# Kernel optimization log

Hardware: AMD Instinct MI355X
Metric: run time of the kernel (lower is better)

The kernel has to match this reference:

```python
import jax, jax.numpy as jnp
import numpy as np

N = 50000   # nodes
E = 600000  # edges (time_feat is per-edge: same mask indexes k and src_idx)
D = 128     # adapter_dim
C = 8       # num_clusters
SCALE = D ** -0.5


def setup_inputs() -> dict:
    key = jax.random.key(0)
    ks = jax.random.split(key, 12)
    s = 1.0 / np.sqrt(D)
    return {
        "node_feat": jax.random.normal(ks[0], (N, D), jnp.float32),
        "time_feat": jax.random.normal(ks[1], (E, D), jnp.float32),
        "context_feat": jax.random.normal(ks[2], (N, D), jnp.float32),
        "edge_index": jax.random.randint(ks[3], (2, E), 0, N),
        "Wq": jax.random.uniform(ks[4], (D, D), jnp.float32, -s, s),
        "bq": jnp.zeros((D,), jnp.float32),
        "Wk": jax.random.uniform(ks[5], (D, D), jnp.float32, -s, s),
        "bk": jnp.zeros((D,), jnp.float32),
        "Wv": jax.random.uniform(ks[6], (D, D), jnp.float32, -s, s),
        "bv": jnp.zeros((D,), jnp.float32),
        "cluster_emb": jax.random.normal(ks[7], (C, D), jnp.float32),
        "Wo": jax.random.uniform(ks[8], (D, D), jnp.float32, -s, s),
        "bo": jnp.zeros((D,), jnp.float32),
    }


def reference(node_feat, time_feat, context_feat, edge_index,
              Wq, bq, Wk, bk, Wv, bv, cluster_emb, Wo, bo):
    q = node_feat @ Wq + bq            # [N, D]
    k = time_feat @ Wk + bk            # [E, D]
    v = time_feat @ Wv + bv            # [E, D]

    # cluster routing: argmax(softmax(sim)) == argmax(sim)
    sim = (time_feat @ cluster_emb.T) * SCALE   # [E, C]
    assign = jnp.argmax(sim, axis=-1)           # [E] int

    src = edge_index[0]                          # [E]
    seg = assign * N + src                       # combined (cluster, dst-of-scatter) segment id
    nseg = C * N

    attn = jnp.sum(q[src] * k, axis=-1) * SCALE  # [E]

    # scatter_softmax per (cluster, src node)
    seg_max = jax.ops.segment_max(attn, seg, num_segments=nseg)
    ex = jnp.exp(attn - seg_max[seg])
    denom = jax.ops.segment_sum(ex, seg, num_segments=nseg)
    w = ex / denom[seg]                          # [E]

    # scatter_mean per (cluster, src node) -> [C, N, D]
    wv = v * w[:, None]
    sums = jax.ops.segment_sum(wv, seg, num_segments=nseg)                 # [C*N, D]
    counts = jax.ops.segment_sum(jnp.ones((E,), v.dtype), seg, num_segments=nseg)
    means = sums / jnp.maximum(counts, 1.0)[:, None]                       # empty -> 0
    per_cluster = means.reshape(C, N, D)

    # sum(outputs) / len(outputs): only non-empty clusters contribute an entry
    edges_per_cluster = jax.ops.segment_sum(jnp.ones((E,), jnp.float32), assign, num_segments=C)
    num_nonempty = jnp.sum((edges_per_cluster > 0).astype(jnp.float32))
    combined = per_cluster.sum(axis=0) / num_nonempty                      # [N, D]

    return jax.nn.relu(combined @ Wo + bo)
```

## Files before the change

### kernel.cpp

```cpp
#include <hip/hip_runtime.h>
#include <math.h>


#define NN 50000
#define NE 600000
#define DD 128
#define NC 8
#define WIN 64
#define NWIN 9376
#define NBF  9377
#define EC 70
#define NLOC 32
#define SCALEF 0.08838834764831845f

#define OFF_NODECNT  0
#define OFF_FILL     50000
#define OFF_MASK     100000
#define ZERO_ELEMS   100256
#define OFF_NODEOFF  100352
#define OFF_PARTIAL  150352
#define OFF_BF       150608
#define OFF_BQK      160000
#define OFF_BVO      160128
#define OFF_WQBK     160256
#define OFF_C0       160384
#define OFF_WQK      160400
#define OFF_WVO      176784
#define OFF_QB       193168
#define OFF_SORTED   243168
#define OFF_SRCS     843168
#define OFF_SW       1443168
#define OFF_P        1493168

__device__ __forceinline__ float dot4(float4 a, float4 b) {
  return a.x * b.x + a.y * b.y + a.z * b.z + a.w * b.w;
}

__global__ __launch_bounds__(256) void k_pre_count(
    const float* __restrict__ Wq, const float* __restrict__ bq,
    const float* __restrict__ Wk, const float* __restrict__ bk,
    const float* __restrict__ Wv, const float* __restrict__ bv,
    const float* __restrict__ Wo, const int* __restrict__ ei,
    int* __restrict__ node_cnt,
    float* __restrict__ Wqk, float* __restrict__ bqk,
    float* __restrict__ Wvo, float* __restrict__ bvo,
    float* __restrict__ wqbk, float* __restrict__ c0) {
  int bid = blockIdx.x, t = threadIdx.x;
  if (bid >= 129) {
    long e = (long)(bid - 129) * 256 + t;
    if (e < NE) atomicAdd(&node_cnt[ei[e]], 1);
    return;
  }
  __shared__ float rq[DD], rv[DD];
  int b = bid;
  if (b < DD) {
    if (t < DD) { rq[t] = Wq[b * DD + t]; rv[t] = Wv[b * DD + t]; }
    __syncthreads();
    if (t < DD) {
      float aq = 0.f, av = 0.f;
      for (int j = 0; j < DD; j++) {
        aq += rq[j] * Wk[t * DD + j];
        av += rv[j] * Wo[j * DD + t];
      }
      Wqk[b * DD + t] = aq;
      Wvo[b * DD + t] = av;
    }
  } else {
    if (t < DD) {
      float a1 = 0.f, a2 = 0.f, a3 = 0.f;
      for (int j = 0; j < DD; j++) {
        a1 += bq[j] * Wk[t * DD + j];
        a2 += bv[j] * Wo[j * DD + t];
        a3 += Wq[t * DD + j] * bk[j];
      }
      bqk[t] = a1; bvo[t] = a2; wqbk[t] = a3;
      if (t == 0) {
        float s = 0.f;
        for (int j = 0; j < DD; j++) s += bq[j] * bk[j];
        *c0 = s;
      }
    }
  }
}

__global__ __launch_bounds__(256) void k_p(
    const float* __restrict__ nf, const float* __restrict__ Wqk,
    const float* __restrict__ bqk, const float* __restrict__ wqbk,
    const float* __restrict__ c0p,
    float* __restrict__ p, float* __restrict__ qb) {
  __shared__ float a_lds[64 * DD];
  __shared__ float wb_lds[DD];
  int t = threadIdx.x;
  long row0 = (long)blockIdx.x * 64;
  for (int it = 0; it < 8; it++) {
    int idx = (it * 256 + t) * 4;
    long r = row0 + idx / DD;
    float4 v = {0.f, 0.f, 0.f, 0.f};
    if (r < NN) v = *(const float4*)(nf + r * DD + (idx % DD));
    *(float4*)(a_lds + idx) = v;
  }
  if (t < DD) wb_lds[t] = wqbk[t];
  __syncthreads();
  int cg = t % 32, rg = t / 32;
  int col0 = cg * 4, r0 = rg * 8;
  float acc[8][4]; float qacc[8];
  for (int r = 0; r < 8; r++) { qacc[r] = 0.f; for (int c = 0; c < 4; c++) acc[r][c] = 0.f; }
  for (int k = 0; k < DD; k++) {
    float4 b4 = *(const float4*)(Wqk + k * DD + col0);
    float wbk = wb_lds[k];
    for (int r = 0; r < 8; r++) {
      float a = a_lds[(r0 + r) * DD + k];
      acc[r][0] += a * b4.x; acc[r][1] += a * b4.y;
      acc[r][2] += a * b4.z; acc[r][3] += a * b4.w;
      qacc[r] += a * wbk;
    }
  }
  float4 bq4 = *(const float4*)(bqk + col0);
  float c0v = *c0p;
  for (int r = 0; r < 8; r++) {
    long row = row0 + r0 + r;
    if (row < NN) {
      float4 o;
      o.x = acc[r][0] + bq4.x; o.y = acc[r][1] + bq4.y;
      o.z = acc[r][2] + bq4.z; o.w = acc[r][3] + bq4.w;
      *(float4*)(p + row * DD + col0) = o;
      if (cg == 0) qb[row] = qacc[r] + c0v;
    }
  }
}

__global__ __launch_bounds__(256) void k_scan1(const int* __restrict__ node_cnt,
                                               int* __restrict__ partial) {
  int i = blockIdx.x * 256 + threadIdx.x;
  int v = (i < NN) ? node_cnt[i] : 0;
  for (int o = 1; o < 64; o <<= 1) v += __shfl_xor(v, o);
  __shared__ int wsum[4];
  if ((threadIdx.x & 63) == 0) wsum[threadIdx.x >> 6] = v;
  __syncthreads();
  if (threadIdx.x == 0) partial[blockIdx.x] = wsum[0] + wsum[1] + wsum[2] + wsum[3];
}

__global__ __launch_bounds__(256) void k_scan2(int* __restrict__ partial) {
  __shared__ int s[256];
  int t = threadIdx.x;
  int v = (t < 196) ? partial[t] : 0;
  s[t] = v;
  __syncthreads();
  for (int o = 1; o < 256; o <<= 1) {
    int add = (t >= o) ? s[t - o] : 0;
    __syncthreads();
    s[t] += add;
    __syncthreads();
  }
  if (t < 196) partial[t] = s[t] - v;
}

__global__ __launch_bounds__(256) void k_scan3(const int* __restrict__ node_cnt,
                                               const int* __restrict__ partial,
                                               int* __restrict__ node_off) {
  __shared__ int s[256];
  int t = threadIdx.x;
  int i = blockIdx.x * 256 + t;
  int v = (i < NN) ? node_cnt[i] : 0;
  s[t] = v;
  __syncthreads();
  for (int o = 1; o < 256; o <<= 1) {
    int add = (t >= o) ? s[t - o] : 0;
    __syncthreads();
    s[t] += add;
    __syncthreads();
  }
  if (i < NN) node_off[i] = partial[blockIdx.x] + s[t] - v;
}

#define EDGE_BLKS 2344
#define BS_BLKS   37
__global__ __launch_bounds__(256) void k_scatter(const int* __restrict__ ei,
                                                 const int* __restrict__ node_off,
                                                 int* __restrict__ fill,
                                                 int* __restrict__ sorted,
                                                 int* __restrict__ srcs,
                                                 int* __restrict__ blockFirst) {
  int bid = blockIdx.x, t = threadIdx.x;
  if (bid >= EDGE_BLKS) {
    int w = (bid - EDGE_BLKS) * 256 + t;
    if (w < NBF) {
      int v = w * WIN, lo = 0, hi = NN;
      while (lo < hi) { int mid = (lo + hi) >> 1; if (node_off[mid] < v) lo = mid + 1; else hi = mid; }
      blockFirst[w] = lo;
    }
    return;
  }
  long e = (long)bid * 256 + t;
  if (e < NE) {
    int s = ei[e];
    int pos = node_off[s] + atomicAdd(&fill[s], 1);
    sorted[pos] = (int)e;
    srcs[pos] = s;
  }
}

__device__ __forceinline__ void phase_a16(
    const float* __restrict__ tf, const float* __restrict__ p,
    const float4 (&ceg)[NC][2], float* t_lds, float* exf_sh, int* cli_sh,
    float* D_sh, int* C_sh,
    int slot, int jA, int eid, int src, int lnode, float qbv,
    bool doStage, bool doDC) {
  const float* trow = tf + (long)eid * DD;
  float4 t0 = *(const float4*)(trow + jA * 4);
  float4 t1 = *(const float4*)(trow + (16 + jA) * 4);
  if (doStage) {
    int e7 = slot & 7;
    *(float4*)(t_lds + slot * DD + ((jA ^ e7) << 2)) = t0;
    *(float4*)(t_lds + slot * DD + ((16 + (jA ^ e7)) << 2)) = t1;
  }
  const float* prow = p + (long)src * DD;
  float4 p0 = *(const float4*)(prow + jA * 4);
  float4 p1 = *(const float4*)(prow + (16 + jA) * 4);
  float a = dot4(t0, p0) + dot4(t1, p1);
  float sims[NC];
  #pragma unroll
  for (int c = 0; c < NC; c++)
    sims[c] = dot4(t0, ceg[c][0]) + dot4(t1, ceg[c][1]);
  #pragma unroll
  for (int c = 0; c < NC; c++) {
    sims[c] += __shfl_xor(sims[c], 1);
    sims[c] += __shfl_xor(sims[c], 2);
    sims[c] += __shfl_xor(sims[c], 4);
    sims[c] += __shfl_xor(sims[c], 8);
  }
  a += __shfl_xor(a, 1);
  a += __shfl_xor(a, 2);
  a += __shfl_xor(a, 4);
  a += __shfl_xor(a, 8);
  if (jA == 0) {
    float best = sims[0]; int bc = 0;
    #pragma unroll
    for (int c = 1; c < NC; c++) if (sims[c] > best) { best = sims[c]; bc = c; }
    float ex = expf((a + qbv) * SCALEF);
    exf_sh[slot] = ex; cli_sh[slot] = bc;
    if (doDC) {
      atomicAdd(&D_sh[lnode * NC + bc], ex);
      atomicAdd(&C_sh[lnode * NC + bc], 1);
    }
  }
}

__global__ __launch_bounds__(256, 4) void k_fused5(
    const float* __restrict__ tf, const int* __restrict__ sorted,
    const int* __restrict__ srcs, const int* __restrict__ node_off,
    const int* __restrict__ node_cnt, const int* __restrict__ blockFirst,
    const float* __restrict__ ce, const float* __restrict__ p,
    const float* __restrict__ qb, int* __restrict__ maskArr,
    float* __restrict__ agg, float* __restrict__ sw) {
  __shared__ float t_lds[EC * DD];
  __shared__ float exf_sh[EC];
  __shared__ float scl_sh[EC];
  __shared__ int   cli_sh[EC];
  __shared__ int   eidx_sh[EC];
  __shared__ int   srcs_sh[EC];
  __shared__ int   offL_sh[NLOC];
  __shared__ int   cntL_sh[NLOC];
  __shared__ float qb_sh[NLOC];
  __shared__ float D_sh[NLOC * NC];
  __shared__ int   C_sh[NLOC * NC];
  __shared__ int   ctrl[4];

  int t = threadIdx.x, b = blockIdx.x;
  int fn = blockFirst[b], ln = blockFirst[b + 1] - 1;
  if (fn >= NN || ln < fn) return;

  int elA = t >> 4, jA = t & 15;
  int team = t >> 5, c4 = t & 31;
  int msk = 0;

  float4 ceg[NC][2];
  #pragma unroll
  for (int c = 0; c < NC; c++) {
    ceg[c][0] = *(const float4*)(ce + c * DD + jA * 4);
    ceg[c][1] = *(const float4*)(ce + c * DD + (16 + jA) * 4);
  }

  int s0 = fn;
  while (s0 <= ln) {
    if (t < 64) {
      int offv = 0, cntv = 0; bool fit = false;
      bool valid = (t < NLOC && s0 + t <= ln);
      if (valid) { offv = node_off[s0 + t]; cntv = node_cnt[s0 + t]; }
      int off0 = __shfl(offv, 0);
      if (valid) {
        fit = (offv - off0 + cntv) <= EC;
        offL_sh[t] = offv - off0; cntL_sh[t] = cntv; qb_sh[t] = qb[s0 + t];
      }
      unsigned long long bm = __ballot(fit);
      int pref = (int)__popcll(bm);
      if (t == 0) { ctrl[0] = pref; ctrl[2] = off0; }
      if (pref > 0 && t == pref - 1) ctrl[1] = offv - off0 + cntv;
    }
    for (int i = t; i < NLOC * NC; i += 256) { D_sh[i] = 0.f; C_sh[i] = 0; }
    __syncthreads();
    int nN = ctrl[0], eb = ctrl[2];

    if (nN == 0) {
      int cnt = cntL_sh[0];
      float qbv0 = qb_sh[0];
      for (int c0 = 0; c0 < cnt; c0 += 16) {
        int el = c0 + elA;
        if (el < cnt)
          phase_a16(tf, p, ceg, t_lds, exf_sh, cli_sh, D_sh, C_sh,
                    elA, jA, sorted[eb + el], s0, 0, qbv0, false, true);
      }
      __syncthreads();
      float4 r = {0.f, 0.f, 0.f, 0.f};
      for (int c0 = 0; c0 < cnt; c0 += EC) {
        int m = cnt - c0; if (m > EC) m = EC;
        for (int r0 = 0; r0 < m; r0 += 16) {
          int sl = r0 + elA;
          if (sl < m)
            phase_a16(tf, p, ceg, t_lds, exf_sh, cli_sh, D_sh, C_sh,
                      sl, jA, sorted[eb + c0 + sl], s0, 0, qbv0, true, false);
        }
        __syncthreads();
        if (t < m) {
          int c = cli_sh[t];
          scl_sh[t] = exf_sh[t] * __builtin_amdgcn_rcpf(D_sh[c] * (float)C_sh[c]);
        }
        __syncthreads();
        for (int e = team; e < m; e += 8) {
          float s = scl_sh[e];
          const float4 tv = *(const float4*)(t_lds + e * DD + ((c4 ^ (e & 7)) << 2));
          r.x += s * tv.x; r.y += s * tv.y; r.z += s * tv.z; r.w += s * tv.w;
        }
        __syncthreads();
      }
      *(float4*)(t_lds + team * DD + c4 * 4) = r;
      __syncthreads();
      if (t < DD) {
        float acc = 0.f;
        #pragma unroll
        for (int tm = 0; tm < 8; tm++) acc += t_lds[tm * DD + t];
        agg[(long)s0 * DD + t] = acc;
      }
      if (t == 0) {
        float ssw = 0.f; int mk = 0;
        #pragma unroll
        for (int c = 0; c < NC; c++) {
          int cc = C_sh[c];
          if (cc > 0) { mk |= 1 << c; ssw += __builtin_amdgcn_rcpf((float)cc); }
        }
        sw[s0] = ssw; msk |= mk;
      }
      __syncthreads();
      s0 += 1;
      continue;
    }

    int span = ctrl[1];

    if (t < span) { eidx_sh[t] = sorted[eb + t]; srcs_sh[t] = srcs[eb + t]; }
    __syncthreads();

    float4 tc0 = {0.f,0.f,0.f,0.f}, tc1 = {0.f,0.f,0.f,0.f};
    if (elA < span) {
      const float* tr = tf + (long)eidx_sh[elA] * DD;
      tc0 = *(const float4*)(tr + jA * 4);
      tc1 = *(const float4*)(tr + (16 + jA) * 4);
    }
    for (int r0 = 0; r0 < span; r0 += 16) {
      int el = r0 + elA;
      int eln = el + 16;
      float4 tn0 = {0.f,0.f,0.f,0.f}, tn1 = {0.f,0.f,0.f,0.f};
      if (eln < span) {
        const float* tr = tf + (long)eidx_sh[eln] * DD;
        tn0 = *(const float4*)(tr + jA * 4);
        tn1 = *(const float4*)(tr + (16 + jA) * 4);
      }
      if (el < span) {
        int src = srcs_sh[el];
        int e7 = el & 7;
        *(float4*)(t_lds + el * DD + ((jA ^ e7) << 2)) = tc0;
        *(float4*)(t_lds + el * DD + ((16 + (jA ^ e7)) << 2)) = tc1;
        const float* prow = p + (long)src * DD;
        float4 p0 = *(const float4*)(prow + jA * 4);
        float4 p1 = *(const float4*)(prow + (16 + jA) * 4);
        float a = dot4(tc0, p0) + dot4(tc1, p1);
        float sims[NC];
        #pragma unroll
        for (int c = 0; c < NC; c++)
          sims[c] = dot4(tc0, ceg[c][0]) + dot4(tc1, ceg[c][1]);
        #pragma unroll
        for (int c = 0; c < NC; c++) {
          sims[c] += __shfl_xor(sims[c], 1);
          sims[c] += __shfl_xor(sims[c], 2);
          sims[c] += __shfl_xor(sims[c], 4);
          sims[c] += __shfl_xor(sims[c], 8);
        }
        a += __shfl_xor(a, 1);
        a += __shfl_xor(a, 2);
        a += __shfl_xor(a, 4);
        a += __shfl_xor(a, 8);
        if (jA == 0) {
          float best = sims[0]; int bc = 0;
          #pragma unroll
          for (int c = 1; c < NC; c++) if (sims[c] > best) { best = sims[c]; bc = c; }
          float ex = expf((a + qb_sh[src - s0]) * SCALEF);
          exf_sh[el] = ex; cli_sh[el] = bc;
          atomicAdd(&D_sh[(src - s0) * NC + bc], ex);
          atomicAdd(&C_sh[(src - s0) * NC + bc], 1);
        }
      }
      tc0 = tn0; tc1 = tn1;
    }
    __syncthreads();

    if (t < span) {
      int l = (srcs_sh[t] - s0) * NC + cli_sh[t];
      scl_sh[t] = exf_sh[t] * __builtin_amdgcn_rcpf(D_sh[l] * (float)C_sh[l]);
    }
    __syncthreads();

    for (int k = team; k < nN; k += 8) {
      float4 r = {0.f, 0.f, 0.f, 0.f};
      int e1 = offL_sh[k] + cntL_sh[k];
      for (int e = offL_sh[k]; e < e1; e++) {
        float s = scl_sh[e];
        const float4 tv = *(const float4*)(t_lds + e * DD + ((c4 ^ (e & 7)) << 2));
        r.x += s * tv.x; r.y += s * tv.y; r.z += s * tv.z; r.w += s * tv.w;
      }
      long n = s0 + k;
      *(float4*)(agg + n * DD + c4 * 4) = r;
      if (c4 == 0) {
        float ssw = 0.f; int mk = 0;
        #pragma unroll
        for (int c = 0; c < NC; c++) {
          int cc = C_sh[k * NC + c];
          if (cc > 0) { mk |= 1 << c; ssw += __builtin_amdgcn_rcpf((float)cc); }
        }
        sw[n] = ssw; msk |= mk;
      }
    }
    __syncthreads();
    s0 += nN;
  }
  if ((t & 31) == 0 && msk) atomicOr(&maskArr[b & 255], msk);
}

__global__ __launch_bounds__(256) void k_out(
    const float* __restrict__ agg, const float* __restrict__ Wvo,
    const float* __restrict__ bvo, const float* __restrict__ sw,
    const float* __restrict__ bo, const int* __restrict__ maskArr,
    float* __restrict__ out) {
  __shared__ float a_lds[64 * DD];
  __shared__ float sw_lds[64];
  __shared__ int morw[4];
  int t = threadIdx.x;
  int mv = maskArr[t];
  for (int o = 1; o < 64; o <<= 1) mv |= __shfl_xor(mv, o);
  if ((t & 63) == 0) morw[t >> 6] = mv;
  long row0 = (long)blockIdx.x * 64;
  for (int it = 0; it < 8; it++) {
    int idx = (it * 256 + t) * 4;
    long r = row0 + idx / DD;
    float4 v = {0.f, 0.f, 0.f, 0.f};
    if (r < NN) v = *(const float4*)(agg + r * DD + (idx % DD));
    *(float4*)(a_lds + idx) = v;
  }
  if (t < 64) {
    long r = row0 + t;
    sw_lds[t] = (r < NN) ? sw[r] : 0.f;
  }
  __syncthreads();
  int full = morw[0] | morw[1] | morw[2] | morw[3];
  int nne = __popc(full); if (nne == 0) nne = 1;
  float inv = 1.0f / (float)nne;
  int cg = t % 32, rg = t / 32;
  int col0 = cg * 4, r0 = rg * 8;
  float acc[8][4];
  for (int r = 0; r < 8; r++) for (int c = 0; c < 4; c++) acc[r][c] = 0.f;
  for (int k = 0; k < DD; k++) {
    float4 b4 = *(const float4*)(Wvo + k * DD + col0);
    for (int r = 0; r < 8; r++) {
      float a = a_lds[(r0 + r) * DD + k];
      acc[r][0] += a * b4.x; acc[r][1] += a * b4.y;
      acc[r][2] += a * b4.z; acc[r][3] += a * b4.w;
    }
  }
  float4 bv4 = *(const float4*)(bvo + col0);
  float4 bo4 = *(const float4*)(bo + col0);
  for (int r = 0; r < 8; r++) {
    long row = row0 + r0 + r;
    if (row < NN) {
      float s = sw_lds[r0 + r];
      float4 o;
      o.x = fmaxf((acc[r][0] + s * bv4.x) * inv + bo4.x, 0.f);
      o.y = fmaxf((acc[r][1] + s * bv4.y) * inv + bo4.y, 0.f);
      o.z = fmaxf((acc[r][2] + s * bv4.z) * inv + bo4.z, 0.f);
      o.w = fmaxf((acc[r][3] + s * bv4.w) * inv + bo4.w, 0.f);
      *(float4*)(out + row * DD + col0) = o;
    }
  }
}

extern "C" void kernel_launch(void* const* d_in, const int* in_sizes, int n_in,
                              void* d_out, int out_size, void* d_ws, size_t ws_size,
                              hipStream_t stream) {
  const float* nf = (const float*)d_in[0];
  const float* tf = (const float*)d_in[1];
  const int*   ei = (const int*)d_in[3];
  const float* Wq = (const float*)d_in[4];
  const float* bq = (const float*)d_in[5];
  const float* Wk = (const float*)d_in[6];
  const float* bk = (const float*)d_in[7];
  const float* Wv = (const float*)d_in[8];
  const float* bv = (const float*)d_in[9];
  const float* ce = (const float*)d_in[10];
  const float* Wo = (const float*)d_in[11];
  const float* bo = (const float*)d_in[12];
  float* out = (float*)d_out;

  float* ws  = (float*)d_ws;
  int*   node_cnt = (int*)(ws + OFF_NODECNT);
  int*   fill     = (int*)(ws + OFF_FILL);
  int*   maskArr  = (int*)(ws + OFF_MASK);
  int*   node_off = (int*)(ws + OFF_NODEOFF);
  int*   partial  = (int*)(ws + OFF_PARTIAL);
  int*   blockFirst = (int*)(ws + OFF_BF);
  float* bqk      = ws + OFF_BQK;
  float* bvo      = ws + OFF_BVO;
  float* wqbk     = ws + OFF_WQBK;
  float* c0       = ws + OFF_C0;
  float* Wqk      = ws + OFF_WQK;
  float* Wvo      = ws + OFF_WVO;
  float* qb       = ws + OFF_QB;
  int*   sorted   = (int*)(ws + OFF_SORTED);
  int*   srcs     = (int*)(ws + OFF_SRCS);
  float* sw       = ws + OFF_SW;
  float* p        = ws + OFF_P;
  float* agg      = ws + OFF_P;

  hipMemsetAsync(d_ws, 0, (size_t)ZERO_ELEMS * 4, stream);

  k_pre_count<<<129 + EDGE_BLKS, 256, 0, stream>>>(
      Wq, bq, Wk, bk, Wv, bv, Wo, ei, node_cnt, Wqk, bqk, Wvo, bvo, wqbk, c0);
  k_p<<<(NN + 63) / 64, 256, 0, stream>>>(nf, Wqk, bqk, wqbk, c0, p, qb);
  k_scan1<<<196, 256, 0, stream>>>(node_cnt, partial);
  k_scan2<<<1, 256, 0, stream>>>(partial);
  k_scan3<<<196, 256, 0, stream>>>(node_cnt, partial, node_off);
  k_scatter<<<EDGE_BLKS + BS_BLKS, 256, 0, stream>>>(ei, node_off, fill, sorted,
                                                     srcs, blockFirst);
  k_fused5<<<NWIN, 256, 0, stream>>>(tf, sorted, srcs, node_off, node_cnt,
                                     blockFirst, ce, p, qb, maskArr, agg, sw);
  k_out<<<(NN + 63) / 64, 256, 0, stream>>>(agg, Wvo, bvo, sw, bo, maskArr, out);
}
```

Before: 666.0 us.

## Stage all edge time-feature rows into LDS upfront and shrink edge windows

```diff
diff --git a/kernel.cpp b/kernel.cpp
--- a/kernel.cpp
+++ b/kernel.cpp
@@ -6,11 +6,11 @@
 #define NE 600000
 #define DD 128
 #define NC 8
-#define WIN 64
-#define NWIN 9376
-#define NBF  9377
+#define WIN 56
+#define NWIN 10715
+#define NBF  10716
 #define EC 70
-#define NLOC 32
+#define NLOC 24
 #define SCALEF 0.08838834764831845f
 
 #define OFF_NODECNT  0
@@ -20,17 +20,17 @@
 #define OFF_NODEOFF  100352
 #define OFF_PARTIAL  150352
 #define OFF_BF       150608
-#define OFF_BQK      160000
-#define OFF_BVO      160128
-#define OFF_WQBK     160256
-#define OFF_C0       160384
-#define OFF_WQK      160400
-#define OFF_WVO      176784
-#define OFF_QB       193168
-#define OFF_SORTED   243168
-#define OFF_SRCS     843168
-#define OFF_SW       1443168
-#define OFF_P        1493168
+#define OFF_BQK      161328
+#define OFF_BVO      161456
+#define OFF_WQBK     161584
+#define OFF_C0       161712
+#define OFF_WQK      161728
+#define OFF_WVO      178112
+#define OFF_QB       194496
+#define OFF_SORTED   244496
+#define OFF_SRCS     844496
+#define OFF_SW       1444496
+#define OFF_P        1494496
 
 __device__ __forceinline__ float dot4(float4 a, float4 b) {
   return a.x * b.x + a.y * b.y + a.z * b.z + a.w * b.w;
@@ -174,7 +174,7 @@
 }
 
 #define EDGE_BLKS 2344
-#define BS_BLKS   37
+#define BS_BLKS   42
 __global__ __launch_bounds__(256) void k_scatter(const int* __restrict__ ei,
                                                  const int* __restrict__ node_off,
                                                  int* __restrict__ fill,
@@ -246,7 +246,7 @@
   }
 }
 
-__global__ __launch_bounds__(256, 4) void k_fused5(
+__global__ __launch_bounds__(256, 4) void k_fused7(
     const float* __restrict__ tf, const int* __restrict__ sorted,
     const int* __restrict__ srcs, const int* __restrict__ node_off,
     const int* __restrict__ node_cnt, const int* __restrict__ blockFirst,
@@ -257,7 +257,6 @@
   __shared__ float exf_sh[EC];
   __shared__ float scl_sh[EC];
   __shared__ int   cli_sh[EC];
-  __shared__ int   eidx_sh[EC];
   __shared__ int   srcs_sh[EC];
   __shared__ int   offL_sh[NLOC];
   __shared__ int   cntL_sh[NLOC];
@@ -272,6 +271,7 @@
 
   int elA = t >> 4, jA = t & 15;
   int team = t >> 5, c4 = t & 31;
+  int rR = t >> 3, cL = t & 7;
   int msk = 0;
 
   float4 ceg[NC][2];
@@ -357,37 +357,41 @@
 
     int span = ctrl[1];
 
-    if (t < span) { eidx_sh[t] = sorted[eb + t]; srcs_sh[t] = srcs[eb + t]; }
-    __syncthreads();
-
-    float4 tc0 = {0.f,0.f,0.f,0.f}, tc1 = {0.f,0.f,0.f,0.f};
-    if (elA < span) {
-      const float* tr = tf + (long)eidx_sh[elA] * DD;
-      tc0 = *(const float4*)(tr + jA * 4);
-      tc1 = *(const float4*)(tr + (16 + jA) * 4);
-    }
+    if (t < span) srcs_sh[t] = srcs[eb + t];
+    for (int base = 0; base < span; base += 32) {
+      int r = base + rR;
+      if (r < span) {
+        const float* tr = tf + (long)sorted[eb + r] * DD;
+        float4 v0 = *(const float4*)(tr + (cL + 0) * 4);
+        float4 v1 = *(const float4*)(tr + (cL + 8) * 4);
+        float4 v2 = *(const float4*)(tr + (cL + 16) * 4);
+        float4 v3 = *(const float4*)(tr + (cL + 24) * 4);
+        int sw8 = r & 7;
+        float* rb = t_lds + r * DD;
+        *(float4*)(rb + (((cL + 0) ^ sw8) << 2)) = v0;
+        *(float4*)(rb + (((cL + 8) ^ sw8) << 2)) = v1;
+        *(float4*)(rb + (((cL + 16) ^ sw8) << 2)) = v2;
+        *(float4*)(rb + (((cL + 24) ^ sw8) << 2)) = v3;
+      }
+    }
+    __syncthreads();
+
     for (int r0 = 0; r0 < span; r0 += 16) {
       int el = r0 + elA;
-      int eln = el + 16;
-      float4 tn0 = {0.f,0.f,0.f,0.f}, tn1 = {0.f,0.f,0.f,0.f};
-      if (eln < span) {
-        const float* tr = tf + (long)eidx_sh[eln] * DD;
-        tn0 = *(const float4*)(tr + jA * 4);
-        tn1 = *(const float4*)(tr + (16 + jA) * 4);
-      }
       if (el < span) {
+        int sw8 = el & 7;
+        const float* rb = t_lds + el * DD;
+        float4 t0 = *(const float4*)(rb + ((jA ^ sw8) << 2));
+        float4 t1 = *(const float4*)(rb + ((16 + (jA ^ sw8)) << 2));
         int src = srcs_sh[el];
-        int e7 = el & 7;
-        *(float4*)(t_lds + el * DD + ((jA ^ e7) << 2)) = tc0;
-        *(float4*)(t_lds + el * DD + ((16 + (jA ^ e7)) << 2)) = tc1;
-        const float* prow = p + (long)src * DD;
-        float4 p0 = *(const float4*)(prow + jA * 4);
-        float4 p1 = *(const float4*)(prow + (16 + jA) * 4);
-        float a = dot4(tc0, p0) + dot4(tc1, p1);
+        const float* pr = p + (long)src * DD;
+        float4 p0 = *(const float4*)(pr + jA * 4);
+        float4 p1 = *(const float4*)(pr + (16 + jA) * 4);
+        float a = dot4(t0, p0) + dot4(t1, p1);
         float sims[NC];
         #pragma unroll
         for (int c = 0; c < NC; c++)
-          sims[c] = dot4(tc0, ceg[c][0]) + dot4(tc1, ceg[c][1]);
+          sims[c] = dot4(t0, ceg[c][0]) + dot4(t1, ceg[c][1]);
         #pragma unroll
         for (int c = 0; c < NC; c++) {
           sims[c] += __shfl_xor(sims[c], 1);
@@ -409,7 +413,6 @@
           atomicAdd(&C_sh[(src - s0) * NC + bc], 1);
         }
       }
-      tc0 = tn0; tc1 = tn1;
     }
     __syncthreads();
 
@@ -548,7 +551,7 @@
   k_scan3<<<196, 256, 0, stream>>>(node_cnt, partial, node_off);
   k_scatter<<<EDGE_BLKS + BS_BLKS, 256, 0, stream>>>(ei, node_off, fill, sorted,
                                                      srcs, blockFirst);
-  k_fused5<<<NWIN, 256, 0, stream>>>(tf, sorted, srcs, node_off, node_cnt,
+  k_fused7<<<NWIN, 256, 0, stream>>>(tf, sorted, srcs, node_off, node_cnt,
                                      blockFirst, ce, p, qb, maskArr, agg, sw);
   k_out<<<(NN + 63) / 64, 256, 0, stream>>>(agg, Wvo, bvo, sw, bo, maskArr, out);
 }
```

Result: slower. 702.3 us (+5.5%).
